# Performance work log

Measured on AMD Instinct MI355X. Metric: run time of the kernel, lower is better.

Reference implementation:

```python
import jax, jax.numpy as jnp
import numpy as np

SIGMA = 1.0

def _pairwise_sqdist(x, y):
    # x: [N,3], y: [M,3] -> [N,M] squared distances via gram expansion
    xx = jnp.sum(x * x, axis=-1)[:, None]
    yy = jnp.sum(y * y, axis=-1)[None, :]
    xy = x @ y.T
    return jnp.maximum(xx + yy - 2.0 * xy, 0.0)

def _cauchy(d2, sigma):
    return 1.0 / (1.0 + d2 / (sigma * sigma))

def setup_inputs() -> dict:
    key = jax.random.key(0)
    k1, k2, k3, k4 = jax.random.split(key, 4)
    V, N, M = 4096, 8192, 8192
    src_vertices = jax.random.normal(k1, (V, 3), dtype=jnp.float32)
    tar_normals = jax.random.normal(k2, (M, 3), dtype=jnp.float32)
    tar_centers = jax.random.normal(k3, (M, 3), dtype=jnp.float32)
    src_indices = jax.random.randint(k4, (N, 3), 0, V)
    return {"src_vertices": src_vertices, "tar_normals": tar_normals,
            "tar_centers": tar_centers, "src_indices": src_indices}

def reference(src_vertices, tar_normals, tar_centers, src_indices):
    # Gather triangle vertices: [N,3(verts),3(xyz)]
    tris = src_vertices[src_indices]
    a, b, c = tris[:, 0, :], tris[:, 1, :], tris[:, 2, :]
    normals = 0.5 * jnp.cross(a - b, c - b)        # [N,3]
    centers = tris.sum(axis=1) / 3.0               # [N,3]

    # Currents energy with cauchy kernel K(x,y) = 1/(1 + |x-y|^2/sigma^2)
    K_ss = _cauchy(_pairwise_sqdist(centers, centers), SIGMA)      # [N,N]
    K_st = _cauchy(_pairwise_sqdist(centers, tar_centers), SIGMA)  # [N,M]
    K_tt = _cauchy(_pairwise_sqdist(tar_centers, tar_centers), SIGMA)  # [M,M]

    e_ss = jnp.sum(K_ss * (normals @ normals.T))
    e_st = jnp.sum(K_st * (normals @ tar_normals.T))
    e_tt = jnp.sum(K_tt * (tar_normals @ tar_normals.T))
    return e_ss - 2.0 * e_st + e_tt
```

## Files before the change

### kernel.cpp

```cpp
#include <hip/hip_runtime.h>

typedef short bf16x8 __attribute__((ext_vector_type(8)));
typedef float f32x16 __attribute__((ext_vector_type(16)));

static __device__ __forceinline__ unsigned short f2bf(float x) {
    unsigned u = __builtin_bit_cast(unsigned, x);
    unsigned r = (u + 0x7FFFu + ((u >> 16) & 1u)) >> 16;
    return (unsigned short)r;
}
static __device__ __forceinline__ float bf2f(unsigned short h) {
    unsigned u = (unsigned)h << 16;
    return __builtin_bit_cast(float, u);
}


__global__ void dc_pack(const float* __restrict__ verts,
                        const float* __restrict__ tnorm,
                        const float* __restrict__ tcent,
                        const int* __restrict__ idx,
                        unsigned short* __restrict__ ws,
                        float* __restrict__ out,
                        int N, int M) {
    int p = blockIdx.x * 64 + threadIdx.x;
    if (p == 0) out[0] = 0.0f;
    int P = N + M;
    if (p >= P) return;

    float cx, cy, cz, nx, ny, nz;
    if (p < N) {
        int i0 = idx[3 * p + 0], i1 = idx[3 * p + 1], i2 = idx[3 * p + 2];
        float ax = verts[3 * i0], ay = verts[3 * i0 + 1], az = verts[3 * i0 + 2];
        float bx = verts[3 * i1], by = verts[3 * i1 + 1], bz = verts[3 * i1 + 2];
        float qx = verts[3 * i2], qy = verts[3 * i2 + 1], qz = verts[3 * i2 + 2];
        float ux = ax - bx, uy = ay - by, uz = az - bz;
        float vx = qx - bx, vy = qy - by, vz = qz - bz;
        nx = 0.5f * (uy * vz - uz * vy);
        ny = 0.5f * (uz * vx - ux * vz);
        nz = 0.5f * (ux * vy - uy * vx);
        cx = (ax + bx + qx) * (1.0f / 3.0f);
        cy = (ay + by + qy) * (1.0f / 3.0f);
        cz = (az + bz + qz) * (1.0f / 3.0f);
    } else {
        int t = p - N;
        cx = tcent[3 * t]; cy = tcent[3 * t + 1]; cz = tcent[3 * t + 2];
        nx = -tnorm[3 * t]; ny = -tnorm[3 * t + 1]; nz = -tnorm[3 * t + 2];
    }

    unsigned short chx = f2bf(cx), chy = f2bf(cy), chz = f2bf(cz);
    unsigned short clx = f2bf(cx - bf2f(chx));
    unsigned short cly = f2bf(cy - bf2f(chy));
    unsigned short clz = f2bf(cz - bf2f(chz));
    unsigned short nhx = f2bf(nx), nhy = f2bf(ny), nhz = f2bf(nz);
    unsigned short nlx = f2bf(nx - bf2f(nhx));
    unsigned short nly = f2bf(ny - bf2f(nhy));
    unsigned short nlz = f2bf(nz - bf2f(nhz));
    float ex = bf2f(chx) + bf2f(clx);
    float ey = bf2f(chy) + bf2f(cly);
    float ez = bf2f(chz) + bf2f(clz);
    float s = ex * ex + ey * ey + ez * ez;
    unsigned short sh = f2bf(s), sl = f2bf(s - bf2f(sh));
    unsigned short m2hx = f2bf(-2.0f * bf2f(chx)), m2hy = f2bf(-2.0f * bf2f(chy)), m2hz = f2bf(-2.0f * bf2f(chz));
    unsigned short m2lx = f2bf(-2.0f * bf2f(clx)), m2ly = f2bf(-2.0f * bf2f(cly)), m2lz = f2bf(-2.0f * bf2f(clz));
    const unsigned short one = 0x3F80;

    __align__(16) unsigned short A1v[16] = {
        m2hx, m2hy, m2hz,  m2hx, m2hy, m2hz,  m2lx, m2ly, m2lz,
        sh, sl,  one, one,  one,  0, 0 };
    __align__(16) unsigned short B1v[16] = {
        chx, chy, chz,  clx, cly, clz,  chx, chy, chz,
        one, one,  sh, sl,  one,  0, 0 };
    __align__(16) unsigned short A2v[16] = {
        nhx, nhy, nhz,  nhx, nhy, nhz,  nlx, nly, nlz,
        0, 0, 0, 0, 0, 0, 0 };
    __align__(16) unsigned short B2v[16] = {
        nhx, nhy, nhz,  nlx, nly, nlz,  nhx, nhy, nhz,
        0, 0, 0, 0, 0, 0, 0 };

    size_t arr = (size_t)P * 16;
    unsigned short* A1 = ws;
    unsigned short* A2 = ws + arr;
    unsigned short* B1 = ws + 2 * arr;
    unsigned short* B2 = ws + 3 * arr;

    int tile = p >> 5, m = p & 31;
    size_t lo = ((size_t)tile * 64 + m) * 8;
    size_t hi = lo + 32 * 8;

    *(uint4*)(A1 + lo) = *(const uint4*)&A1v[0];
    *(uint4*)(A1 + hi) = *(const uint4*)&A1v[8];
    *(uint4*)(A2 + lo) = *(const uint4*)&A2v[0];
    *(uint4*)(A2 + hi) = *(const uint4*)&A2v[8];
    *(uint4*)(B1 + lo) = *(const uint4*)&B1v[0];
    *(uint4*)(B1 + hi) = *(const uint4*)&B1v[8];
    *(uint4*)(B2 + lo) = *(const uint4*)&B2v[0];
    *(uint4*)(B2 + hi) = *(const uint4*)&B2v[8];
}

static __device__ __forceinline__ void acc8(float2& part, const f32x16& d1, const f32x16& d2) {
#pragma unroll
    for (int g = 0; g < 2; ++g) {
        const int r = 8 * g;
        float p01 = d1[r + 0] * d1[r + 1];
        float p23 = d1[r + 2] * d1[r + 3];
        float p45 = d1[r + 4] * d1[r + 5];
        float p67 = d1[r + 6] * d1[r + 7];
        float n01 = fmaf(d2[r + 0], d1[r + 1], d2[r + 1] * d1[r + 0]);
        float n23 = fmaf(d2[r + 2], d1[r + 3], d2[r + 3] * d1[r + 2]);
        float n45 = fmaf(d2[r + 4], d1[r + 5], d2[r + 5] * d1[r + 4]);
        float n67 = fmaf(d2[r + 6], d1[r + 7], d2[r + 7] * d1[r + 6]);
        float q03 = p01 * p23;
        float q47 = p45 * p67;
        float m03 = fmaf(n01, p23, n23 * p01);
        float m47 = fmaf(n45, p67, n67 * p45);
        float T   = q03 * q47;
        float NUM = fmaf(m03, q47, m47 * q03);
        (&part.x)[g] = fmaf(NUM, __builtin_amdgcn_rcpf(T), (&part.x)[g]);
    }
}

__global__ __launch_bounds__(1024, 4) void dc_pair_mfma(
    const unsigned short* __restrict__ ws, float* __restrict__ out, int P) {
    __shared__ float wsum[16];

    const int nT = P >> 5;
    size_t arr = (size_t)P * 16;
    const unsigned short* A1 = ws;
    const unsigned short* A2 = ws + arr;
    const unsigned short* B1 = ws + 2 * arr;
    const unsigned short* B2 = ws + 3 * arr;

    int tid = threadIdx.x;
    int lane = tid & 63, wv = tid >> 6;
    int gi = blockIdx.x * 16 + wv;
    int rp = gi >> 4, c = gi & 15;
    int I0 = 2 * rp, I1 = I0 + 1;

    const size_t lo = (size_t)lane * 8;

    bf16x8 a1_0 = *(const bf16x8*)(A1 + (size_t)I0 * 512 + lo);
    bf16x8 a2_0 = *(const bf16x8*)(A2 + (size_t)I0 * 512 + lo);
    bf16x8 a1_1 = *(const bf16x8*)(A1 + (size_t)I1 * 512 + lo);
    bf16x8 a2_1 = *(const bf16x8*)(A2 + (size_t)I1 * 512 + lo);

    const f32x16 zero = {0.f,0.f,0.f,0.f,0.f,0.f,0.f,0.f,0.f,0.f,0.f,0.f,0.f,0.f,0.f,0.f};
    float2 partA = make_float2(0.f, 0.f);
    float2 corrP = make_float2(0.f, 0.f);
    float2 corrM = make_float2(0.f, 0.f);

    auto wrap = [&](int j) -> size_t {
        return (size_t)(j >= nT ? j - nT : j) * 512;
    };
    auto process = [&](const bf16x8& b1, const bf16x8& b2) {
        f32x16 d1 = __builtin_amdgcn_mfma_f32_32x32x16_bf16(a1_0, b1, zero, 0, 0, 0);
        f32x16 d2 = __builtin_amdgcn_mfma_f32_32x32x16_bf16(a2_0, b2, zero, 0, 0, 0);
        acc8(partA, d1, d2);
        f32x16 e1 = __builtin_amdgcn_mfma_f32_32x32x16_bf16(a1_1, b1, zero, 0, 0, 0);
        f32x16 e2 = __builtin_amdgcn_mfma_f32_32x32x16_bf16(a2_1, b2, zero, 0, 0, 0);
        acc8(partA, e1, e2);
    };
    auto one_tile = [&](float2& part, const bf16x8& x1, const bf16x8& x2, int jm) {
        const bf16x8 b1 = *(const bf16x8*)(B1 + (size_t)jm * 512 + lo);
        const bf16x8 b2 = *(const bf16x8*)(B2 + (size_t)jm * 512 + lo);
        f32x16 d1 = __builtin_amdgcn_mfma_f32_32x32x16_bf16(x1, b1, zero, 0, 0, 0);
        f32x16 d2 = __builtin_amdgcn_mfma_f32_32x32x16_bf16(x2, b2, zero, 0, 0, 0);
        acc8(part, d1, d2);
    };

    int js = I0 + 1 + 16 * c;

    bf16x8 bA1 = *(const bf16x8*)(B1 + wrap(js) + lo);
    bf16x8 bA2 = *(const bf16x8*)(B2 + wrap(js) + lo);
#pragma unroll 1
    for (int it = 0; it < 16; it += 2) {
        size_t o1 = wrap(js + it + 1);
        bf16x8 bB1 = *(const bf16x8*)(B1 + o1 + lo);
        bf16x8 bB2 = *(const bf16x8*)(B2 + o1 + lo);
        process(bA1, bA2);
        size_t o2 = wrap(js + it + 2);
        bA1 = *(const bf16x8*)(B1 + o2 + lo);
        bA2 = *(const bf16x8*)(B2 + o2 + lo);
        process(bB1, bB2);
    }

    if (c == 0) {
        one_tile(corrP, a1_0, a2_0, I0);
        one_tile(corrM, a1_1, a2_1, I0 + 1);
    } else if (c == 15) {
        int v = I0 + 256; if (v >= nT) v -= nT;
        int y = I0 + 257; if (y >= nT) y -= nT;
        one_tile(corrM, a1_0, a2_0, v);
        one_tile(corrP, a1_1, a2_1, y);
    }

    float s = 2.0f * (partA.x + partA.y)
            + (corrP.x + corrP.y)
            - (corrM.x + corrM.y);
#pragma unroll
    for (int off = 32; off > 0; off >>= 1) s += __shfl_down(s, off, 64);
    if (lane == 0) wsum[wv] = s;
    __syncthreads();
    if (tid == 0) {
        float t = 0.f;
#pragma unroll
        for (int i = 0; i < 16; ++i) t += wsum[i];
        atomicAdd(out, t);
    }
}

extern "C" void kernel_launch(void* const* d_in, const int* in_sizes, int n_in,
                              void* d_out, int out_size, void* d_ws, size_t ws_size,
                              hipStream_t stream) {
    const float* verts = (const float*)d_in[0];
    const float* tnorm = (const float*)d_in[1];
    const float* tcent = (const float*)d_in[2];
    const int*   sidx  = (const int*)d_in[3];

    int M = in_sizes[1] / 3;
    int N = in_sizes[3] / 3;
    int P = N + M;

    unsigned short* ws = (unsigned short*)d_ws;
    float* out = (float*)d_out;

    int pblocks = (P + 63) / 64;
    dc_pack<<<pblocks, 64, 0, stream>>>(verts, tnorm, tcent, sidx, ws, out, N, M);

    dc_pair_mfma<<<256, 1024, 0, stream>>>(ws, out, P);
}
```

Measured before the change: 81.15 us.

## Fuse pack and pairwise kernels into one cooperative launch with grid sync

Merges the packing kernel into the pairwise MFMA kernel. Wave 0 of each of the 256 blocks packs 64 points (256*64 = 16384 = P), and a grid-wide cooperative sync then separates packing from the pairwise phase. This removes one kernel launch and the gap between the two launches. In exchange it adds grid-sync overhead, depends on all 256 blocks of 1024 threads being co-resident, and the pack coverage only holds when P <= 16384.

After: 192.1 us. 137% more time.

```diff
diff --git a/kernel.cpp b/kernel.cpp
--- a/kernel.cpp
+++ b/kernel.cpp
@@ -1,4 +1,7 @@
 #include <hip/hip_runtime.h>
+#include <hip/hip_cooperative_groups.h>
+
+namespace cg = cooperative_groups;
 
 typedef short bf16x8 __attribute__((ext_vector_type(8)));
 typedef float f32x16 __attribute__((ext_vector_type(16)));
@@ -11,89 +14,6 @@
 static __device__ __forceinline__ float bf2f(unsigned short h) {
     unsigned u = (unsigned)h << 16;
     return __builtin_bit_cast(float, u);
-}
-
-
-__global__ void dc_pack(const float* __restrict__ verts,
-                        const float* __restrict__ tnorm,
-                        const float* __restrict__ tcent,
-                        const int* __restrict__ idx,
-                        unsigned short* __restrict__ ws,
-                        float* __restrict__ out,
-                        int N, int M) {
-    int p = blockIdx.x * 64 + threadIdx.x;
-    if (p == 0) out[0] = 0.0f;
-    int P = N + M;
-    if (p >= P) return;
-
-    float cx, cy, cz, nx, ny, nz;
-    if (p < N) {
-        int i0 = idx[3 * p + 0], i1 = idx[3 * p + 1], i2 = idx[3 * p + 2];
-        float ax = verts[3 * i0], ay = verts[3 * i0 + 1], az = verts[3 * i0 + 2];
-        float bx = verts[3 * i1], by = verts[3 * i1 + 1], bz = verts[3 * i1 + 2];
-        float qx = verts[3 * i2], qy = verts[3 * i2 + 1], qz = verts[3 * i2 + 2];
-        float ux = ax - bx, uy = ay - by, uz = az - bz;
-        float vx = qx - bx, vy = qy - by, vz = qz - bz;
-        nx = 0.5f * (uy * vz - uz * vy);
-        ny = 0.5f * (uz * vx - ux * vz);
-        nz = 0.5f * (ux * vy - uy * vx);
-        cx = (ax + bx + qx) * (1.0f / 3.0f);
-        cy = (ay + by + qy) * (1.0f / 3.0f);
-        cz = (az + bz + qz) * (1.0f / 3.0f);
-    } else {
-        int t = p - N;
-        cx = tcent[3 * t]; cy = tcent[3 * t + 1]; cz = tcent[3 * t + 2];
-        nx = -tnorm[3 * t]; ny = -tnorm[3 * t + 1]; nz = -tnorm[3 * t + 2];
-    }
-
-    unsigned short chx = f2bf(cx), chy = f2bf(cy), chz = f2bf(cz);
-    unsigned short clx = f2bf(cx - bf2f(chx));
-    unsigned short cly = f2bf(cy - bf2f(chy));
-    unsigned short clz = f2bf(cz - bf2f(chz));
-    unsigned short nhx = f2bf(nx), nhy = f2bf(ny), nhz = f2bf(nz);
-    unsigned short nlx = f2bf(nx - bf2f(nhx));
-    unsigned short nly = f2bf(ny - bf2f(nhy));
-    unsigned short nlz = f2bf(nz - bf2f(nhz));
-    float ex = bf2f(chx) + bf2f(clx);
-    float ey = bf2f(chy) + bf2f(cly);
-    float ez = bf2f(chz) + bf2f(clz);
-    float s = ex * ex + ey * ey + ez * ez;
-    unsigned short sh = f2bf(s), sl = f2bf(s - bf2f(sh));
-    unsigned short m2hx = f2bf(-2.0f * bf2f(chx)), m2hy = f2bf(-2.0f * bf2f(chy)), m2hz = f2bf(-2.0f * bf2f(chz));
-    unsigned short m2lx = f2bf(-2.0f * bf2f(clx)), m2ly = f2bf(-2.0f * bf2f(cly)), m2lz = f2bf(-2.0f * bf2f(clz));
-    const unsigned short one = 0x3F80;
-
-    __align__(16) unsigned short A1v[16] = {
-        m2hx, m2hy, m2hz,  m2hx, m2hy, m2hz,  m2lx, m2ly, m2lz,
-        sh, sl,  one, one,  one,  0, 0 };
-    __align__(16) unsigned short B1v[16] = {
-        chx, chy, chz,  clx, cly, clz,  chx, chy, chz,
-        one, one,  sh, sl,  one,  0, 0 };
-    __align__(16) unsigned short A2v[16] = {
-        nhx, nhy, nhz,  nhx, nhy, nhz,  nlx, nly, nlz,
-        0, 0, 0, 0, 0, 0, 0 };
-    __align__(16) unsigned short B2v[16] = {
-        nhx, nhy, nhz,  nlx, nly, nlz,  nhx, nhy, nhz,
-        0, 0, 0, 0, 0, 0, 0 };
-
-    size_t arr = (size_t)P * 16;
-    unsigned short* A1 = ws;
-    unsigned short* A2 = ws + arr;
-    unsigned short* B1 = ws + 2 * arr;
-    unsigned short* B2 = ws + 3 * arr;
-
-    int tile = p >> 5, m = p & 31;
-    size_t lo = ((size_t)tile * 64 + m) * 8;
-    size_t hi = lo + 32 * 8;
-
-    *(uint4*)(A1 + lo) = *(const uint4*)&A1v[0];
-    *(uint4*)(A1 + hi) = *(const uint4*)&A1v[8];
-    *(uint4*)(A2 + lo) = *(const uint4*)&A2v[0];
-    *(uint4*)(A2 + hi) = *(const uint4*)&A2v[8];
-    *(uint4*)(B1 + lo) = *(const uint4*)&B1v[0];
-    *(uint4*)(B1 + hi) = *(const uint4*)&B1v[8];
-    *(uint4*)(B2 + lo) = *(const uint4*)&B2v[0];
-    *(uint4*)(B2 + hi) = *(const uint4*)&B2v[8];
 }
 
 static __device__ __forceinline__ void acc8(float2& part, const f32x16& d1, const f32x16& d2) {
@@ -118,19 +38,99 @@
     }
 }
 
-__global__ __launch_bounds__(1024, 4) void dc_pair_mfma(
-    const unsigned short* __restrict__ ws, float* __restrict__ out, int P) {
+__global__ __launch_bounds__(1024, 4) void dc_fused(
+    const float* __restrict__ verts,
+    const float* __restrict__ tnorm,
+    const float* __restrict__ tcent,
+    const int* __restrict__ idx,
+    unsigned short* __restrict__ ws,
+    float* __restrict__ out,
+    int N, int M) {
     __shared__ float wsum[16];
 
+    const int P = N + M;
     const int nT = P >> 5;
     size_t arr = (size_t)P * 16;
-    const unsigned short* A1 = ws;
-    const unsigned short* A2 = ws + arr;
-    const unsigned short* B1 = ws + 2 * arr;
-    const unsigned short* B2 = ws + 3 * arr;
+    unsigned short* A1 = ws;
+    unsigned short* A2 = ws + arr;
+    unsigned short* B1 = ws + 2 * arr;
+    unsigned short* B2 = ws + 3 * arr;
 
     int tid = threadIdx.x;
     int lane = tid & 63, wv = tid >> 6;
+
+    if (wv == 0) {
+        int p = blockIdx.x * 64 + lane;
+        if (p == 0) out[0] = 0.0f;
+        if (p < P) {
+            float cx, cy, cz, nx, ny, nz;
+            if (p < N) {
+                int i0 = idx[3 * p + 0], i1 = idx[3 * p + 1], i2 = idx[3 * p + 2];
+                float ax = verts[3 * i0], ay = verts[3 * i0 + 1], az = verts[3 * i0 + 2];
+                float bx = verts[3 * i1], by = verts[3 * i1 + 1], bz = verts[3 * i1 + 2];
+                float qx = verts[3 * i2], qy = verts[3 * i2 + 1], qz = verts[3 * i2 + 2];
+                float ux = ax - bx, uy = ay - by, uz = az - bz;
+                float vx = qx - bx, vy = qy - by, vz = qz - bz;
+                nx = 0.5f * (uy * vz - uz * vy);
+                ny = 0.5f * (uz * vx - ux * vz);
+                nz = 0.5f * (ux * vy - uy * vx);
+                cx = (ax + bx + qx) * (1.0f / 3.0f);
+                cy = (ay + by + qy) * (1.0f / 3.0f);
+                cz = (az + bz + qz) * (1.0f / 3.0f);
+            } else {
+                int t = p - N;
+                cx = tcent[3 * t]; cy = tcent[3 * t + 1]; cz = tcent[3 * t + 2];
+                nx = -tnorm[3 * t]; ny = -tnorm[3 * t + 1]; nz = -tnorm[3 * t + 2];
+            }
+
+            unsigned short chx = f2bf(cx), chy = f2bf(cy), chz = f2bf(cz);
+            unsigned short clx = f2bf(cx - bf2f(chx));
+            unsigned short cly = f2bf(cy - bf2f(chy));
+            unsigned short clz = f2bf(cz - bf2f(chz));
+            unsigned short nhx = f2bf(nx), nhy = f2bf(ny), nhz = f2bf(nz);
+            unsigned short nlx = f2bf(nx - bf2f(nhx));
+            unsigned short nly = f2bf(ny - bf2f(nhy));
+            unsigned short nlz = f2bf(nz - bf2f(nhz));
+            float ex = bf2f(chx) + bf2f(clx);
+            float ey = bf2f(chy) + bf2f(cly);
+            float ez = bf2f(chz) + bf2f(clz);
+            float s = ex * ex + ey * ey + ez * ez;
+            unsigned short sh = f2bf(s), sl = f2bf(s - bf2f(sh));
+            unsigned short m2hx = f2bf(-2.0f * bf2f(chx)), m2hy = f2bf(-2.0f * bf2f(chy)), m2hz = f2bf(-2.0f * bf2f(chz));
+            unsigned short m2lx = f2bf(-2.0f * bf2f(clx)), m2ly = f2bf(-2.0f * bf2f(cly)), m2lz = f2bf(-2.0f * bf2f(clz));
+            const unsigned short one = 0x3F80;
+
+            __align__(16) unsigned short A1v[16] = {
+                m2hx, m2hy, m2hz,  m2hx, m2hy, m2hz,  m2lx, m2ly, m2lz,
+                sh, sl,  one, one,  one,  0, 0 };
+            __align__(16) unsigned short B1v[16] = {
+                chx, chy, chz,  clx, cly, clz,  chx, chy, chz,
+                one, one,  sh, sl,  one,  0, 0 };
+            __align__(16) unsigned short A2v[16] = {
+                nhx, nhy, nhz,  nhx, nhy, nhz,  nlx, nly, nlz,
+                0, 0, 0, 0, 0, 0, 0 };
+            __align__(16) unsigned short B2v[16] = {
+                nhx, nhy, nhz,  nlx, nly, nlz,  nhx, nhy, nhz,
+                0, 0, 0, 0, 0, 0, 0 };
+
+            int tile = p >> 5, m = p & 31;
+            size_t plo = ((size_t)tile * 64 + m) * 8;
+            size_t phi = plo + 32 * 8;
+
+            *(uint4*)(A1 + plo) = *(const uint4*)&A1v[0];
+            *(uint4*)(A1 + phi) = *(const uint4*)&A1v[8];
+            *(uint4*)(A2 + plo) = *(const uint4*)&A2v[0];
+            *(uint4*)(A2 + phi) = *(const uint4*)&A2v[8];
+            *(uint4*)(B1 + plo) = *(const uint4*)&B1v[0];
+            *(uint4*)(B1 + phi) = *(const uint4*)&B1v[8];
+            *(uint4*)(B2 + plo) = *(const uint4*)&B2v[0];
+            *(uint4*)(B2 + phi) = *(const uint4*)&B2v[8];
+        }
+    }
+
+    __threadfence();
+    cg::this_grid().sync();
+
     int gi = blockIdx.x * 16 + wv;
     int rp = gi >> 4, c = gi & 15;
     int I0 = 2 * rp, I1 = I0 + 1;
@@ -217,13 +217,12 @@
 
     int M = in_sizes[1] / 3;
     int N = in_sizes[3] / 3;
-    int P = N + M;
 
     unsigned short* ws = (unsigned short*)d_ws;
     float* out = (float*)d_out;
 
-    int pblocks = (P + 63) / 64;
-    dc_pack<<<pblocks, 64, 0, stream>>>(verts, tnorm, tcent, sidx, ws, out, N, M);
-
-    dc_pair_mfma<<<256, 1024, 0, stream>>>(ws, out, P);
-}
+    void* args[] = { (void*)&verts, (void*)&tnorm, (void*)&tcent, (void*)&sidx,
+                     (void*)&ws, (void*)&out, (void*)&N, (void*)&M };
+    hipLaunchCooperativeKernel((void*)dc_fused, dim3(256), dim3(1024),
+                               args, 0, stream);
+}
```
